# Optimization experiments

Hardware: AMD Instinct MI355X
Metric: run time of the kernel (lower is better)

## Reference

```python
import jax, jax.numpy as jnp
import numpy as np

H, W = 256, 512          # hdri_resolution
HW = H * W
NPR, NSR = 512, 8        # num primary rays, num_secondary_rays
NUM_ENVS = 1
HDRI_ANGLE = 0.0         # degrees


def _direction_map(h, w):
    # matches equirectangular_range_to_direction(u/W, v/H), range = [2pi, -pi, pi, 0]
    v = (np.arange(h, dtype=np.float64) / h)[:, None]
    u = (np.arange(w, dtype=np.float64) / w)[None, :]
    phi = 2.0 * np.pi * u - np.pi            # [1, W] -> broadcast [H, W]
    theta = np.pi * v                        # [H, 1]
    sin_t = np.sin(theta)
    x = sin_t * np.cos(phi)
    y = sin_t * np.sin(phi)
    z = np.cos(theta) * np.ones_like(phi)
    return np.stack([x, y, z], axis=-1).astype(np.float32)  # [H, W, 3]


def setup_inputs() -> dict:
    key = jax.random.key(0)
    k1, k2, k3, k4 = jax.random.split(key, 4)
    env_idxs = jax.random.randint(k1, (NPR,), 0, NUM_ENVS, dtype=jnp.int32)
    normal = jax.random.normal(k2, (NPR, 3), dtype=jnp.float32)
    normal = normal / jnp.linalg.norm(normal, axis=1, keepdims=True)
    envs = 1.5 * jax.random.uniform(k3, (NUM_ENVS, H, W, 3), dtype=jnp.float32)  # exposure-scaled HDRI
    direction_map = jnp.asarray(_direction_map(H, W))
    ps_samples = jax.random.uniform(k4, (NPR, NSR, 1), dtype=jnp.float32)
    return {"normal": normal, "envs": envs, "direction_map": direction_map,
            "ps_samples": ps_samples, "env_idxs": env_idxs}


def reference(normal, envs, direction_map, ps_samples, env_idxs):
    dt = normal.dtype
    rot = jnp.array([[1.0, 0.0, 0.0], [0.0, 0.0, -1.0], [0.0, -1.0, 0.0]], dtype=dt)
    rad = HDRI_ANGLE * np.pi / 180.0
    rotz = jnp.array([[np.cos(rad), np.sin(rad), 0.0],
                      [-np.sin(rad), np.cos(rad), 0.0],
                      [0.0, 0.0, 1.0]], dtype=dt)
    # (rotz @ rot @ normal.T).T == normal @ (rotz @ rot).T
    normal_r = normal @ (rotz @ rot).T                                 # [npr, 3]

    intens = jnp.linalg.norm(envs, axis=3).reshape(NUM_ENVS, HW)      # [E, HW]
    intens_b = intens[env_idxs]                                        # [npr, HW]

    dirs = direction_map.reshape(HW, 3)                                # [HW, 3]
    mod = jnp.clip(jnp.einsum('pc,nc->pn', normal_r, dirs), 0.0, 1.0)  # [npr, HW]

    modulated = intens_b * mod                                         # [npr, HW]
    norm_p = modulated / jnp.sum(modulated, axis=1, keepdims=True)     # [npr, HW]
    cdf = jnp.cumsum(norm_p, axis=1)                                   # [npr, HW]

    ps = ps_samples[..., 0]                                            # [npr, nsr]
    # argmax(ps < cdf) over last axis == first idx with cdf > ps == searchsorted right
    choices = jax.vmap(lambda c, p: jnp.searchsorted(c, p, side='right'))(cdf, ps)
    choices = jnp.clip(choices, 0, HW - 1)                             # [npr, nsr]

    Vs = choices // W
    Us = choices % W

    qx = jnp.take_along_axis(norm_p, choices, axis=1) + 1e-7           # [npr, nsr]
    px = 2.0 / HW
    mpx = px * jnp.take_along_axis(mod, choices, axis=1)               # [npr, nsr]
    ratio = mpx / qx                                                   # [npr, nsr]
    return (Vs, Us, ratio)
```

## Files before the change

### kernel.cpp

```cpp
#include <hip/hip_runtime.h>
#include <math.h>

#define HH 256
#define WW 512
#define HWN (HH * WW)
#define NPR 512
#define NSR 8
#define CHUNK 512
#define NCHUNK 256
#define RPB 8
#define CPB 4

__global__ __launch_bounds__(256)
void pack_kernel(const float4* __restrict__ envs4,
                 const float4* __restrict__ dir4,
                 float4* __restrict__ packed) {
    int q = blockIdx.x * blockDim.x + threadIdx.x;
    float4 e0 = envs4[3 * q + 0], e1 = envs4[3 * q + 1], e2 = envs4[3 * q + 2];
    float4 d0 = dir4[3 * q + 0],  d1 = dir4[3 * q + 1],  d2 = dir4[3 * q + 2];
    float i0 = sqrtf(e0.x * e0.x + e0.y * e0.y + e0.z * e0.z);
    float i1 = sqrtf(e0.w * e0.w + e1.x * e1.x + e1.y * e1.y);
    float i2 = sqrtf(e1.z * e1.z + e1.w * e1.w + e2.x * e2.x);
    float i3 = sqrtf(e2.y * e2.y + e2.z * e2.z + e2.w * e2.w);
    packed[4 * q + 0] = make_float4(d0.x, d0.y, d0.z, i0);
    packed[4 * q + 1] = make_float4(d0.w, d1.x, d1.y, i1);
    packed[4 * q + 2] = make_float4(d1.z, d1.w, d2.x, i2);
    packed[4 * q + 3] = make_float4(d2.y, d2.z, d2.w, i3);
}

__global__ __launch_bounds__(256)
void chunksum_kernel(const float* __restrict__ normal,
                     const float4* __restrict__ packed,
                     double* __restrict__ S) {
    const int wave = threadIdx.x >> 6;
    const int lane = threadIdx.x & 63;
    const int c  = blockIdx.x * CPB + wave;
    const int r0 = blockIdx.y * RPB;

    float rx[RPB], ry[RPB], rz[RPB];
#pragma unroll
    for (int i = 0; i < RPB; ++i) {
        int r = r0 + i;
        rx[i] =  normal[3 * r + 0];
        ry[i] = -normal[3 * r + 2];
        rz[i] = -normal[3 * r + 1];
    }

    float acc[RPB];
#pragma unroll
    for (int i = 0; i < RPB; ++i) acc[i] = 0.0f;

    const int base = c * CHUNK + lane;
#pragma unroll
    for (int k = 0; k < CHUNK / 64; ++k) {
        float4 d = packed[base + k * 64];
#pragma unroll
        for (int i = 0; i < RPB; ++i) {
            float m = fmaf(rx[i], d.x, fmaf(ry[i], d.y, rz[i] * d.z));
            m = fminf(fmaxf(m, 0.0f), 1.0f);
            acc[i] = fmaf(d.w, m, acc[i]);
        }
    }

#pragma unroll
    for (int i = 0; i < RPB; ++i) {
        double a = (double)acc[i];
#pragma unroll
        for (int off = 32; off > 0; off >>= 1)
            a += __shfl_down(a, off);
        if (lane == 0) S[(r0 + i) * NCHUNK + c] = a;
    }
}

__global__ __launch_bounds__(256)
void sample_kernel(const float* __restrict__ normal,
                   const float4* __restrict__ packed,
                   const double* __restrict__ S,
                   const float* __restrict__ ps,
                   float* __restrict__ out) {
    const int p = blockIdx.x;
    const int t = threadIdx.x;
    const int wave = t >> 6;
    const int lane = t & 63;

    const float nx = normal[3 * p + 0];
    const float ny = normal[3 * p + 1];
    const float nz = normal[3 * p + 2];
    const float rx = nx, ry = -nz, rz = -ny;

    __shared__ double pref[NCHUNK];
    __shared__ double wsum[4];

    double v = S[p * NCHUNK + t];
    double sc = v;
#pragma unroll
    for (int off = 1; off < 64; off <<= 1) {
        double u = __shfl_up(sc, off);
        if (lane >= off) sc += u;
    }
    if (lane == 63) wsum[wave] = sc;
    __syncthreads();
    double add = 0.0;
    for (int w2 = 0; w2 < wave; ++w2) add += wsum[w2];
    pref[t] = sc + add;
    __syncthreads();

    const double total = pref[NCHUNK - 1];
    const float totalF = (float)total;
    const float px = 2.0f / (float)HWN;

    for (int si = 0; si < 2; ++si) {
        const int s = wave + si * 4;
        const double target = (double)ps[p * NSR + s] * total;

        int lo = 0, hi = NCHUNK;
        while (lo < hi) {
            int mid = (lo + hi) >> 1;
            if (pref[mid] > target) hi = mid; else lo = mid + 1;
        }
        const int c = lo;

        if (c >= NCHUNK) {
            if (lane == 0) {
                int ch = HWN - 1;
                float4 d = packed[ch];
                float m = fmaf(rx, d.x, fmaf(ry, d.y, rz * d.z));
                m = fminf(fmaxf(m, 0.0f), 1.0f);
                float modu = d.w * m;
                float qx = modu / totalF + 1e-7f;
                float ratio = px * m / qx;
                int o = p * NSR + s;
                out[o] = (float)(ch / WW);
                out[NPR * NSR + o] = (float)(ch % WW);
                out[2 * NPR * NSR + o] = ratio;
            }
            continue;
        }

        const double basePref = (c > 0) ? pref[c - 1] : 0.0;
        const int cbase = c * CHUNK;
        const int n0 = cbase + lane * 8;

        float mvals[8];
        float modv[8];
        double lsum = 0.0;
#pragma unroll
        for (int j = 0; j < 8; ++j) {
            float4 d = packed[n0 + j];
            float m = fmaf(rx, d.x, fmaf(ry, d.y, rz * d.z));
            m = fminf(fmaxf(m, 0.0f), 1.0f);
            modv[j] = m;
            mvals[j] = d.w * m;
            lsum += (double)mvals[j];
        }

        double sc2 = lsum;
#pragma unroll
        for (int off = 1; off < 64; off <<= 1) {
            double u = __shfl_up(sc2, off);
            if (lane >= off) sc2 += u;
        }
        double cum = basePref + (sc2 - lsum);

        int myidx = HWN;
        float mymod = 0.0f, mymodu = 0.0f;
#pragma unroll
        for (int j = 0; j < 8; ++j) {
            cum += (double)mvals[j];
            if (cum > target) { myidx = n0 + j; mymod = modv[j]; mymodu = mvals[j]; break; }
        }

        int widx = myidx;
        float wmod = mymod, wmodu = mymodu;
#pragma unroll
        for (int off = 32; off > 0; off >>= 1) {
            int oi = __shfl_down(widx, off);
            float om = __shfl_down(wmod, off);
            float ou = __shfl_down(wmodu, off);
            if (oi < widx) { widx = oi; wmod = om; wmodu = ou; }
        }

        if (lane == 0) {
            int ch = widx;
            if (ch >= HWN) {
                ch = cbase + CHUNK - 1;
                float4 d = packed[ch];
                float m = fmaf(rx, d.x, fmaf(ry, d.y, rz * d.z));
                m = fminf(fmaxf(m, 0.0f), 1.0f);
                wmod = m;
                wmodu = d.w * m;
            }
            float qx = wmodu / totalF + 1e-7f;
            float ratio = px * wmod / qx;
            int o = p * NSR + s;
            out[o] = (float)(ch / WW);
            out[NPR * NSR + o] = (float)(ch % WW);
            out[2 * NPR * NSR + o] = ratio;
        }
    }
}

extern "C" void kernel_launch(void* const* d_in, const int* in_sizes, int n_in,
                              void* d_out, int out_size, void* d_ws, size_t ws_size,
                              hipStream_t stream) {
    const float* normal  = (const float*)d_in[0];
    const float* envs    = (const float*)d_in[1];
    const float* dirmap  = (const float*)d_in[2];
    const float* ps      = (const float*)d_in[3];
    float* out = (float*)d_out;

    float4* packed = (float4*)d_ws;
    double* S      = (double*)((char*)d_ws + (size_t)HWN * 16);

    pack_kernel<<<HWN / 4 / 256, 256, 0, stream>>>(
        (const float4*)envs, (const float4*)dirmap, packed);
    chunksum_kernel<<<dim3(NCHUNK / CPB, NPR / RPB), 256, 0, stream>>>(
        normal, packed, S);
    sample_kernel<<<NPR, 256, 0, stream>>>(normal, packed, S, ps, out);
}
```

Measured before the change: 93.37 us.

## Remove pack kernel and read envs/direction map directly in chunk and sample kernels

Drops the separate pack pass and has both the chunk-sum and sampling kernels load the raw env and direction-map arrays, recomputing intensity in place. Each lane now handles two interleaved 4-element granules, and the in-chunk scan is reworked for that layout. Rows per block are doubled to 16 so the extra sqrt and load work is spread over more rays. This removes one launch and the packed-buffer round trip, but intensity is now recomputed redundantly per row-block and register pressure rises.

Result: faster. 91.36 us (-2.1%).

```diff
diff --git a/kernel.cpp b/kernel.cpp
--- a/kernel.cpp
+++ b/kernel.cpp
@@ -8,29 +8,30 @@
 #define NSR 8
 #define CHUNK 512
 #define NCHUNK 256
-#define RPB 8
+#define RPB 16
 #define CPB 4
 
-__global__ __launch_bounds__(256)
-void pack_kernel(const float4* __restrict__ envs4,
-                 const float4* __restrict__ dir4,
-                 float4* __restrict__ packed) {
-    int q = blockIdx.x * blockDim.x + threadIdx.x;
-    float4 e0 = envs4[3 * q + 0], e1 = envs4[3 * q + 1], e2 = envs4[3 * q + 2];
-    float4 d0 = dir4[3 * q + 0],  d1 = dir4[3 * q + 1],  d2 = dir4[3 * q + 2];
-    float i0 = sqrtf(e0.x * e0.x + e0.y * e0.y + e0.z * e0.z);
-    float i1 = sqrtf(e0.w * e0.w + e1.x * e1.x + e1.y * e1.y);
-    float i2 = sqrtf(e1.z * e1.z + e1.w * e1.w + e2.x * e2.x);
-    float i3 = sqrtf(e2.y * e2.y + e2.z * e2.z + e2.w * e2.w);
-    packed[4 * q + 0] = make_float4(d0.x, d0.y, d0.z, i0);
-    packed[4 * q + 1] = make_float4(d0.w, d1.x, d1.y, i1);
-    packed[4 * q + 2] = make_float4(d1.z, d1.w, d2.x, i2);
-    packed[4 * q + 3] = make_float4(d2.y, d2.z, d2.w, i3);
+__device__ __forceinline__ void load_granule4(const float4* __restrict__ envs4,
+                                              const float4* __restrict__ dir4,
+                                              int f4base,
+                                              float inten[4], float dx[4],
+                                              float dy[4], float dz[4]) {
+    float4 e0 = envs4[f4base + 0], e1 = envs4[f4base + 1], e2 = envs4[f4base + 2];
+    float4 d0 = dir4[f4base + 0],  d1 = dir4[f4base + 1],  d2 = dir4[f4base + 2];
+    inten[0] = sqrtf(e0.x * e0.x + e0.y * e0.y + e0.z * e0.z);
+    inten[1] = sqrtf(e0.w * e0.w + e1.x * e1.x + e1.y * e1.y);
+    inten[2] = sqrtf(e1.z * e1.z + e1.w * e1.w + e2.x * e2.x);
+    inten[3] = sqrtf(e2.y * e2.y + e2.z * e2.z + e2.w * e2.w);
+    dx[0] = d0.x; dy[0] = d0.y; dz[0] = d0.z;
+    dx[1] = d0.w; dy[1] = d1.x; dz[1] = d1.y;
+    dx[2] = d1.z; dy[2] = d1.w; dz[2] = d2.x;
+    dx[3] = d2.y; dy[3] = d2.z; dz[3] = d2.w;
 }
 
 __global__ __launch_bounds__(256)
 void chunksum_kernel(const float* __restrict__ normal,
-                     const float4* __restrict__ packed,
+                     const float4* __restrict__ envs4,
+                     const float4* __restrict__ dir4,
                      double* __restrict__ S) {
     const int wave = threadIdx.x >> 6;
     const int lane = threadIdx.x & 63;
@@ -50,15 +51,19 @@
 #pragma unroll
     for (int i = 0; i < RPB; ++i) acc[i] = 0.0f;
 
-    const int base = c * CHUNK + lane;
-#pragma unroll
-    for (int k = 0; k < CHUNK / 64; ++k) {
-        float4 d = packed[base + k * 64];
-#pragma unroll
-        for (int i = 0; i < RPB; ++i) {
-            float m = fmaf(rx[i], d.x, fmaf(ry[i], d.y, rz[i] * d.z));
-            m = fminf(fmaxf(m, 0.0f), 1.0f);
-            acc[i] = fmaf(d.w, m, acc[i]);
+#pragma unroll
+    for (int g = 0; g < 2; ++g) {
+        const int f4base = c * 384 + g * 192 + 3 * lane;
+        float inten[4], dx[4], dy[4], dz[4];
+        load_granule4(envs4, dir4, f4base, inten, dx, dy, dz);
+#pragma unroll
+        for (int j = 0; j < 4; ++j) {
+#pragma unroll
+            for (int i = 0; i < RPB; ++i) {
+                float m = fmaf(rx[i], dx[j], fmaf(ry[i], dy[j], rz[i] * dz[j]));
+                m = fminf(fmaxf(m, 0.0f), 1.0f);
+                acc[i] = fmaf(inten[j], m, acc[i]);
+            }
         }
     }
 
@@ -74,7 +79,8 @@
 
 __global__ __launch_bounds__(256)
 void sample_kernel(const float* __restrict__ normal,
-                   const float4* __restrict__ packed,
+                   const float4* __restrict__ envs4,
+                   const float4* __restrict__ dir4,
                    const double* __restrict__ S,
                    const float* __restrict__ ps,
                    float* __restrict__ out) {
@@ -82,11 +88,12 @@
     const int t = threadIdx.x;
     const int wave = t >> 6;
     const int lane = t & 63;
-
-    const float nx = normal[3 * p + 0];
-    const float ny = normal[3 * p + 1];
-    const float nz = normal[3 * p + 2];
-    const float rx = nx, ry = -nz, rz = -ny;
+    const float* envs = (const float*)envs4;
+    const float* dirm = (const float*)dir4;
+
+    const float rx =  normal[3 * p + 0];
+    const float ry = -normal[3 * p + 2];
+    const float rz = -normal[3 * p + 1];
 
     __shared__ double pref[NCHUNK];
     __shared__ double wsum[4];
@@ -123,10 +130,11 @@
         if (c >= NCHUNK) {
             if (lane == 0) {
                 int ch = HWN - 1;
-                float4 d = packed[ch];
-                float m = fmaf(rx, d.x, fmaf(ry, d.y, rz * d.z));
-                m = fminf(fmaxf(m, 0.0f), 1.0f);
-                float modu = d.w * m;
+                float ex = envs[3 * ch], ey = envs[3 * ch + 1], ez = envs[3 * ch + 2];
+                float inten = sqrtf(ex * ex + ey * ey + ez * ez);
+                float m = fmaf(rx, dirm[3 * ch], fmaf(ry, dirm[3 * ch + 1], rz * dirm[3 * ch + 2]));
+                m = fminf(fmaxf(m, 0.0f), 1.0f);
+                float modu = inten * m;
                 float qx = modu / totalF + 1e-7f;
                 float ratio = px * m / qx;
                 int o = p * NSR + s;
@@ -139,35 +147,52 @@
 
         const double basePref = (c > 0) ? pref[c - 1] : 0.0;
         const int cbase = c * CHUNK;
-        const int n0 = cbase + lane * 8;
-
-        float mvals[8];
-        float modv[8];
-        double lsum = 0.0;
-#pragma unroll
-        for (int j = 0; j < 8; ++j) {
-            float4 d = packed[n0 + j];
-            float m = fmaf(rx, d.x, fmaf(ry, d.y, rz * d.z));
-            m = fminf(fmaxf(m, 0.0f), 1.0f);
-            modv[j] = m;
-            mvals[j] = d.w * m;
-            lsum += (double)mvals[j];
-        }
-
-        double sc2 = lsum;
+
+        float mvals[8], modv[8];
+        double lsum[2];
+#pragma unroll
+        for (int g = 0; g < 2; ++g) {
+            const int f4base = c * 384 + g * 192 + 3 * lane;
+            float inten[4], dx[4], dy[4], dz[4];
+            load_granule4(envs4, dir4, f4base, inten, dx, dy, dz);
+            double ls = 0.0;
+#pragma unroll
+            for (int j = 0; j < 4; ++j) {
+                float m = fmaf(rx, dx[j], fmaf(ry, dy[j], rz * dz[j]));
+                m = fminf(fmaxf(m, 0.0f), 1.0f);
+                modv[4 * g + j] = m;
+                mvals[4 * g + j] = inten[j] * m;
+                ls += (double)mvals[4 * g + j];
+            }
+            lsum[g] = ls;
+        }
+
+        double s0 = lsum[0], s1 = lsum[1];
 #pragma unroll
         for (int off = 1; off < 64; off <<= 1) {
-            double u = __shfl_up(sc2, off);
-            if (lane >= off) sc2 += u;
-        }
-        double cum = basePref + (sc2 - lsum);
+            double u0 = __shfl_up(s0, off);
+            double u1 = __shfl_up(s1, off);
+            if (lane >= off) { s0 += u0; s1 += u1; }
+        }
+        const double g0tot = __shfl(s0, 63);
+        const double cum0base = basePref + (s0 - lsum[0]);
+        const double cum1base = basePref + g0tot + (s1 - lsum[1]);
 
         int myidx = HWN;
         float mymod = 0.0f, mymodu = 0.0f;
-#pragma unroll
-        for (int j = 0; j < 8; ++j) {
+        double cum = cum0base;
+#pragma unroll
+        for (int j = 0; j < 4 && myidx == HWN; ++j) {
             cum += (double)mvals[j];
-            if (cum > target) { myidx = n0 + j; mymod = modv[j]; mymodu = mvals[j]; break; }
+            if (cum > target) { myidx = cbase + 4 * lane + j; mymod = modv[j]; mymodu = mvals[j]; }
+        }
+        if (myidx == HWN) {
+            cum = cum1base;
+#pragma unroll
+            for (int j = 0; j < 4 && myidx == HWN; ++j) {
+                cum += (double)mvals[4 + j];
+                if (cum > target) { myidx = cbase + 256 + 4 * lane + j; mymod = modv[4 + j]; mymodu = mvals[4 + j]; }
+            }
         }
 
         int widx = myidx;
@@ -184,11 +209,12 @@
             int ch = widx;
             if (ch >= HWN) {
                 ch = cbase + CHUNK - 1;
-                float4 d = packed[ch];
-                float m = fmaf(rx, d.x, fmaf(ry, d.y, rz * d.z));
+                float ex = envs[3 * ch], ey = envs[3 * ch + 1], ez = envs[3 * ch + 2];
+                float inten = sqrtf(ex * ex + ey * ey + ez * ez);
+                float m = fmaf(rx, dirm[3 * ch], fmaf(ry, dirm[3 * ch + 1], rz * dirm[3 * ch + 2]));
                 m = fminf(fmaxf(m, 0.0f), 1.0f);
                 wmod = m;
-                wmodu = d.w * m;
+                wmodu = inten * m;
             }
             float qx = wmodu / totalF + 1e-7f;
             float ratio = px * wmod / qx;
@@ -209,12 +235,10 @@
     const float* ps      = (const float*)d_in[3];
     float* out = (float*)d_out;
 
-    float4* packed = (float4*)d_ws;
-    double* S      = (double*)((char*)d_ws + (size_t)HWN * 16);
-
-    pack_kernel<<<HWN / 4 / 256, 256, 0, stream>>>(
-        (const float4*)envs, (const float4*)dirmap, packed);
+    double* S = (double*)d_ws;
+
     chunksum_kernel<<<dim3(NCHUNK / CPB, NPR / RPB), 256, 0, stream>>>(
-        normal, packed, S);
-    sample_kernel<<<NPR, 256, 0, stream>>>(normal, packed, S, ps, out);
-}
+        normal, (const float4*)envs, (const float4*)dirmap, S);
+    sample_kernel<<<NPR, 256, 0, stream>>>(
+        normal, (const float4*)envs, (const float4*)dirmap, S, ps, out);
+}
```
